# Performance work log

Measured on AMD Instinct MI355X. Metric: run time of the kernel, lower is better.

The kernel has to match this reference:

```python
import jax, jax.numpy as jnp
import numpy as np

N1 = 50000
N2 = 50000
NN = 16
NI = 64
ND = 128


def setup_inputs() -> dict:
    key = jax.random.key(0)
    ks = jax.random.split(key, 12)
    inp = {
        "features1": jax.random.normal(ks[0], (N1, NI), dtype=jnp.float32),
        "features2": jax.random.normal(ks[1], (N2, NI), dtype=jnp.float32),
        "x1": jax.random.normal(ks[2], (N1, 3), dtype=jnp.float32),
        "x2": jax.random.normal(ks[3], (N2, 3), dtype=jnp.float32),
        "nuv1": jax.random.normal(ks[4], (N1, 3, 3), dtype=jnp.float32),
        "nuv2": jax.random.normal(ks[5], (N2, 3, 3), dtype=jnp.float32),
        "topk": jax.random.randint(ks[6], (N1, NN), 0, N2, dtype=jnp.int64),
        # query_f params: Linear(2*Ni, Nd) -> ELU -> Linear(Nd, Nd) -> ELU
        "W1": jax.random.normal(ks[7], (2 * NI, ND), dtype=jnp.float32) * (1.0 / np.sqrt(2 * NI)),
        "b1": jnp.zeros((ND,), dtype=jnp.float32),
        "W2": jax.random.normal(ks[8], (ND, ND), dtype=jnp.float32) * (1.0 / np.sqrt(ND)),
        "b2": jnp.zeros((ND,), dtype=jnp.float32),
        "radius": jnp.float32(1.0),
    }
    return inp


def reference(features1, features2, x1, x2, nuv1, nuv2, topk, W1, b1, W2, b2, radius):
    # gather neighbor features: [N1, nn, Ni]
    feats_nn = features2[topk]
    # concat with self features broadcast over neighbor axis: [N1, nn, 2*Ni]
    feat_self = jnp.broadcast_to(features1[:, None, :], feats_nn.shape)
    h = jnp.concatenate([feats_nn, feat_self], axis=-1)
    # small fused MLP (query_f)
    h = jax.nn.elu(h @ W1 + b1)
    h = jax.nn.elu(h @ W2 + b2)  # [N1, nn, Nd]
    # distance-weighted aggregation
    x_nn = x2[topk]                          # [N1, nn, 3]
    orient = x_nn - x1[:, None, :]
    dis2 = jnp.sum(orient * orient, axis=2)  # [N1, nn]
    w = jnp.exp(-dis2 / (2.0 * radius * radius))
    w = jnp.where(topk == 0, jnp.float32(0.0), w)  # mask padded (index-0) neighbors
    # weighted matmul reduction: [N1, Nd]
    out = jnp.einsum("nk,nkd->nd", w, h)
    return out
```

## Files before the change

### kernel.cpp

```cpp
#include <hip/hip_runtime.h>

#define N1C 50000
#define N2C 50000
#define NNC 16
#define NIC 64
#define NDC 128
#define QB  16
#define MR  256
#define FELEMS (N1C * NIC)

typedef __bf16 bf16x8 __attribute__((ext_vector_type(8)));
typedef float f32x4 __attribute__((ext_vector_type(4)));
typedef unsigned u32x4 __attribute__((ext_vector_type(4)));

#if defined(__has_builtin)
#if __has_builtin(__builtin_amdgcn_cvt_pk_bf16_f32)
#define HAVE_PK_BF16 1
#endif
#if __has_builtin(__builtin_amdgcn_permlane32_swap)
#define HAVE_PL32 1
#endif
#endif

#ifdef HAVE_PK_BF16
typedef __bf16 bf16x2 __attribute__((ext_vector_type(2)));
static __device__ __forceinline__ unsigned int pkbf(float a, float b) {
    bf16x2 r = __builtin_amdgcn_cvt_pk_bf16_f32(a, b);
    return __builtin_bit_cast(unsigned int, r);
}
#else
static __device__ __forceinline__ unsigned short f2bf_sw(float f) {
    unsigned int u = __builtin_bit_cast(unsigned int, f);
    u += 0x7fffu + ((u >> 16) & 1u);
    return (unsigned short)(u >> 16);
}
static __device__ __forceinline__ unsigned int pkbf(float a, float b) {
    return (unsigned int)f2bf_sw(a) | ((unsigned int)f2bf_sw(b) << 16);
}
#endif

static __device__ __forceinline__ float elu(float x) {
    return x > 0.f ? x : __expf(x) - 1.f;
}

static __device__ __forceinline__ void stage16(const uint4* gsrc_lane, uint4* ldst_base) {
#if defined(__has_builtin) && __has_builtin(__builtin_amdgcn_global_load_lds)
    __builtin_amdgcn_global_load_lds(
        (const __attribute__((address_space(1))) void*)gsrc_lane,
        (__attribute__((address_space(3))) void*)ldst_base, 16, 0, 0);
#else
    ldst_base[threadIdx.x & 63] = *gsrc_lane;
#endif
}

__global__ void prep_all(const float* __restrict__ f1, const float* __restrict__ f2,
                         const float* __restrict__ W1, const float* __restrict__ W2,
                         unsigned short* __restrict__ fdst,
                         unsigned short* __restrict__ wsW) {
    const int blk = blockIdx.x;
    if (blk < 3125) {
        const int g = blk * 256 + threadIdx.x;
        const size_t base = (size_t)g * 8;
        const float* src = (base < FELEMS) ? (f1 + base) : (f2 + base - FELEMS);
        const float4 v0 = *(const float4*)src;
        const float4 v1 = *(const float4*)(src + 4);
        uint4 o;
        o.x = pkbf(v0.x, v0.y);
        o.y = pkbf(v0.z, v0.w);
        o.z = pkbf(v1.x, v1.y);
        o.w = pkbf(v1.z, v1.w);
        *(uint4*)(fdst + base) = o;
    } else {
        const int idx  = (blk - 3125) * 256 + threadIdx.x;
        const int m    = idx >> 14;
        const int o    = idx & 16383;
        const int j    = o & 7;
        const int lane = (o >> 3) & 63;
        const int ksmt = o >> 9;
        const int ks   = ksmt & 3;
        const int mt   = ksmt >> 2;
        const int d = mt * 16 + (lane & 15);
        const int k = ks * 32 + (lane >> 4) * 8 + j;
        const float* W = m ? W2 : W1;
        wsW[idx] = (unsigned short)pkbf(W[(size_t)k * NDC + d], 0.f);
    }
}

__global__ __launch_bounds__(512, 4)
void fused_knn_mlp(const unsigned short* __restrict__ f1b,
                   const unsigned short* __restrict__ f2b,
                   const float* __restrict__ x1,
                   const float* __restrict__ x2,
                   const int*   __restrict__ topk,
                   const float* __restrict__ b1,
                   const float* __restrict__ b2,
                   const float* __restrict__ radius,
                   const unsigned short* __restrict__ wsW,
                   float* __restrict__ out)
{
    __shared__ uint4 sW[4096];

    const int tid  = threadIdx.x;
    const int blk  = blockIdx.x;
    const int lane = tid & 63;
    const int wave = tid >> 6;
    const int quad = lane >> 4;
    const int l16  = lane & 15;
    const int rloc = wave * 32 + l16;

    const uint4* wp = (const uint4*)wsW;

    #pragma unroll
    for (int it = 0; it < 8; ++it) {
        const int base = wave * 512 + it * 64;
        stage16(wp + base + lane, sW + base);
    }

    const int idx0 = topk[blk * MR + rloc];
    const int idx1 = topk[blk * MR + rloc + 16];
    const int q0   = blk * QB + wave * 2;
    const int q1   = q0 + 1;

    uint4 xf0[4], xf1[4];
    #pragma unroll
    for (int ks = 0; ks < 2; ++ks) {
        xf0[ks] = *(const uint4*)(f2b + (size_t)idx0 * NIC + ks * 32 + quad * 8);
        xf1[ks] = *(const uint4*)(f2b + (size_t)idx1 * NIC + ks * 32 + quad * 8);
        xf0[ks + 2] = *(const uint4*)(f1b + (size_t)q0 * NIC + ks * 32 + quad * 8);
        xf1[ks + 2] = *(const uint4*)(f1b + (size_t)q1 * NIC + ks * 32 + quad * 8);
    }

    float wg0, wg1;
    {
        const float rr = radius[0];
        const float inv2r2 = 1.f / (2.f * rr * rr);
        const float dx0 = x2[idx0 * 3 + 0] - x1[q0 * 3 + 0];
        const float dy0 = x2[idx0 * 3 + 1] - x1[q0 * 3 + 1];
        const float dz0 = x2[idx0 * 3 + 2] - x1[q0 * 3 + 2];
        const float dx1 = x2[idx1 * 3 + 0] - x1[q1 * 3 + 0];
        const float dy1 = x2[idx1 * 3 + 1] - x1[q1 * 3 + 1];
        const float dz1 = x2[idx1 * 3 + 2] - x1[q1 * 3 + 2];
        wg0 = (idx0 == 0) ? 0.f : __expf(-(dx0 * dx0 + dy0 * dy0 + dz0 * dz0) * inv2r2);
        wg1 = (idx1 == 0) ? 0.f : __expf(-(dx1 * dx1 + dy1 * dy1 + dz1 * dz1) * inv2r2);
    }

    __syncthreads();

    unsigned P[8][2][2];
    #pragma unroll
    for (int mp = 0; mp < 4; ++mp) {
        f32x4 accp[2][2];
        #pragma unroll
        for (int mi = 0; mi < 2; ++mi) {
            const float4 b1v = *(const float4*)(b1 + (mp * 2 + mi) * 16 + quad * 4);
            accp[mi][0] = (f32x4){b1v.x, b1v.y, b1v.z, b1v.w};
            accp[mi][1] = accp[mi][0];
        }
        #pragma unroll
        for (int ks = 0; ks < 4; ++ks) {
            const bf16x8 x0  = __builtin_bit_cast(bf16x8, xf0[ks]);
            const bf16x8 x1v = __builtin_bit_cast(bf16x8, xf1[ks]);
            #pragma unroll
            for (int mi = 0; mi < 2; ++mi) {
                const int mt = mp * 2 + mi;
                const bf16x8 a = *(const bf16x8*)&sW[(mt * 4 + ks) * 64 + lane];
                accp[mi][0] = __builtin_amdgcn_mfma_f32_16x16x32_bf16(a, x0,  accp[mi][0], 0, 0, 0);
                accp[mi][1] = __builtin_amdgcn_mfma_f32_16x16x32_bf16(a, x1v, accp[mi][1], 0, 0, 0);
            }
        }
        #pragma unroll
        for (int mi = 0; mi < 2; ++mi) {
            const int mt = mp * 2 + mi;
            #pragma unroll
            for (int nt = 0; nt < 2; ++nt) {
                P[mt][nt][0] = pkbf(elu(accp[mi][nt][0]), elu(accp[mi][nt][1]));
                P[mt][nt][1] = pkbf(elu(accp[mi][nt][2]), elu(accp[mi][nt][3]));
            }
        }
    }

    f32x4 acc2[2][8];
    #pragma unroll
    for (int nt2 = 0; nt2 < 8; ++nt2) {
        const float bb = b2[nt2 * 16 + l16];
        acc2[0][nt2] = (f32x4){bb, bb, bb, bb};
        acc2[1][nt2] = acc2[0][nt2];
    }
    const bool qodd = (quad & 1) != 0;
    #pragma unroll
    for (int ks = 0; ks < 4; ++ks) {
        u32x4 a2[2];
        #pragma unroll
        for (int mt2 = 0; mt2 < 2; ++mt2) {
#ifdef HAVE_PL32
            #pragma unroll
            for (int e = 0; e < 2; ++e) {
                auto pr = __builtin_amdgcn_permlane32_swap(
                    P[2 * ks][mt2][e], P[2 * ks + 1][mt2][e], false, false);
                const unsigned Rv = qodd ? (unsigned)pr[1] : (unsigned)pr[0];
                const unsigned Zv = qodd ? (unsigned)pr[0] : (unsigned)pr[1];
                const unsigned Sv = __shfl_xor(Zv, 16, 64);
                a2[mt2][e]     = qodd ? Sv : Rv;
                a2[mt2][2 + e] = qodd ? Rv : Sv;
            }
#else
            #pragma unroll
            for (int u = 0; u < 4; ++u) {
                const int src = (((quad * 2) + (u >> 1)) & 3) * 16 + l16;
                const unsigned lo = __shfl(P[2 * ks][mt2][u & 1], src, 64);
                const unsigned hi = __shfl(P[2 * ks + 1][mt2][u & 1], src, 64);
                a2[mt2][u] = (quad & 2) ? hi : lo;
            }
#endif
        }
        const bf16x8 af0 = __builtin_bit_cast(bf16x8, a2[0]);
        const bf16x8 af1 = __builtin_bit_cast(bf16x8, a2[1]);
        #pragma unroll
        for (int nt2 = 0; nt2 < 8; ++nt2) {
            const bf16x8 b = *(const bf16x8*)&sW[2048 + (nt2 * 4 + ks) * 64 + lane];
            acc2[0][nt2] = __builtin_amdgcn_mfma_f32_16x16x32_bf16(af0, b, acc2[0][nt2], 0, 0, 0);
            acc2[1][nt2] = __builtin_amdgcn_mfma_f32_16x16x32_bf16(af1, b, acc2[1][nt2], 0, 0, 0);
        }
    }

    float wk0[4], wk1[4];
    #pragma unroll
    for (int reg = 0; reg < 4; ++reg) {
        const int src = (lane & 48) | (quad * 4 + reg);
        wk0[reg] = __shfl(wg0, src, 64);
        wk1[reg] = __shfl(wg1, src, 64);
    }
    #pragma unroll
    for (int mt2 = 0; mt2 < 2; ++mt2) {
        #pragma unroll
        for (int nt2 = 0; nt2 < 8; ++nt2) {
            const int d2 = nt2 * 16 + l16;
            float s;
            if (mt2 == 0)
                s = elu(acc2[0][nt2][0]) * wk0[0] + elu(acc2[0][nt2][1]) * wk0[1]
                  + elu(acc2[0][nt2][2]) * wk0[2] + elu(acc2[0][nt2][3]) * wk0[3];
            else
                s = elu(acc2[1][nt2][0]) * wk1[0] + elu(acc2[1][nt2][1]) * wk1[1]
                  + elu(acc2[1][nt2][2]) * wk1[2] + elu(acc2[1][nt2][3]) * wk1[3];
            s += __shfl_xor(s, 16, 64);
            s += __shfl_xor(s, 32, 64);
            if (lane < 16) {
                out[(size_t)(blk * QB + wave * 2 + mt2) * NDC + d2] = s;
            }
        }
    }
}

extern "C" void kernel_launch(void* const* d_in, const int* in_sizes, int n_in,
                              void* d_out, int out_size, void* d_ws, size_t ws_size,
                              hipStream_t stream) {
    const float* features1 = (const float*)d_in[0];
    const float* features2 = (const float*)d_in[1];
    const float* x1        = (const float*)d_in[2];
    const float* x2        = (const float*)d_in[3];
    const int*   topk      = (const int*)d_in[6];
    const float* W1        = (const float*)d_in[7];
    const float* b1        = (const float*)d_in[8];
    const float* W2        = (const float*)d_in[9];
    const float* b2        = (const float*)d_in[10];
    const float* radius    = (const float*)d_in[11];
    float* out = (float*)d_out;

    unsigned short* wsW = (unsigned short*)d_ws;
    unsigned short* f1b = wsW + 32768;
    unsigned short* f2b = f1b + FELEMS;

    prep_all<<<dim3(3253), 256, 0, stream>>>(features1, features2, W1, W2, f1b, wsW);
    fused_knn_mlp<<<dim3(N1C / QB), 512, 0, stream>>>(f1b, f2b, x1, x2, topk,
                                                      b1, b2, radius, wsW, out);
}
```

Measured before the change: 187.1 us.

## Make fused kernel persistent with next-tile prefetch and MFMA-based weighted reduction

Turns the fused KNN-MLP kernel into a persistent grid of 512 blocks that loops over query tiles. W1/W2 are staged into LDS once per block, and the next tile's topk indices, gathered features and distance weights load while the current tile runs its MLP. The final weighted sum over neighbours moves from ELU-multiply plus cross-lane shuffle reductions to an fp16 MFMA with the weights as the A operand. This cuts per-block setup and hides gather latency, but lowers occupancy and puts the weights and activations into fp16 for the final reduction.

After: 726.3 us. +288.1%, slower.

```diff
diff --git a/kernel.cpp b/kernel.cpp
--- a/kernel.cpp
+++ b/kernel.cpp
@@ -7,11 +7,16 @@
 #define NDC 128
 #define QB  16
 #define MR  256
+#define NT  (N1C / QB)
+#define PGRID 512
 #define FELEMS (N1C * NIC)
 
 typedef __bf16 bf16x8 __attribute__((ext_vector_type(8)));
 typedef float f32x4 __attribute__((ext_vector_type(4)));
 typedef unsigned u32x4 __attribute__((ext_vector_type(4)));
+typedef unsigned u32x2 __attribute__((ext_vector_type(2)));
+typedef __fp16 f16x4 __attribute__((ext_vector_type(4)));
+typedef __fp16 f16x2 __attribute__((ext_vector_type(2)));
 
 #if defined(__has_builtin)
 #if __has_builtin(__builtin_amdgcn_cvt_pk_bf16_f32)
@@ -19,6 +24,9 @@
 #endif
 #if __has_builtin(__builtin_amdgcn_permlane32_swap)
 #define HAVE_PL32 1
+#endif
+#if __has_builtin(__builtin_amdgcn_mfma_f32_16x16x16f16) && __has_builtin(__builtin_amdgcn_cvt_pkrtz)
+#define HAVE_RED_MFMA 1
 #endif
 #endif
 
@@ -36,6 +44,17 @@
 }
 static __device__ __forceinline__ unsigned int pkbf(float a, float b) {
     return (unsigned int)f2bf_sw(a) | ((unsigned int)f2bf_sw(b) << 16);
+}
+#endif
+
+#ifdef HAVE_RED_MFMA
+static __device__ __forceinline__ unsigned pkh(float a, float b) {
+    f16x2 h = __builtin_amdgcn_cvt_pkrtz(a, b);
+    return __builtin_bit_cast(unsigned, h);
+}
+static __device__ __forceinline__ f16x4 mkf16x4(unsigned lo, unsigned hi) {
+    u32x2 u = {lo, hi};
+    return __builtin_bit_cast(f16x4, u);
 }
 #endif
 
@@ -116,138 +135,201 @@
         stage16(wp + base + lane, sW + base);
     }
 
-    const int idx0 = topk[blk * MR + rloc];
-    const int idx1 = topk[blk * MR + rloc + 16];
-    const int q0   = blk * QB + wave * 2;
-    const int q1   = q0 + 1;
-
+    const float rr = radius[0];
+    const float inv2r2 = 1.f / (2.f * rr * rr);
+
+    int t = blk;
     uint4 xf0[4], xf1[4];
-    #pragma unroll
-    for (int ks = 0; ks < 2; ++ks) {
-        xf0[ks] = *(const uint4*)(f2b + (size_t)idx0 * NIC + ks * 32 + quad * 8);
-        xf1[ks] = *(const uint4*)(f2b + (size_t)idx1 * NIC + ks * 32 + quad * 8);
-        xf0[ks + 2] = *(const uint4*)(f1b + (size_t)q0 * NIC + ks * 32 + quad * 8);
-        xf1[ks + 2] = *(const uint4*)(f1b + (size_t)q1 * NIC + ks * 32 + quad * 8);
-    }
-
     float wg0, wg1;
     {
-        const float rr = radius[0];
-        const float inv2r2 = 1.f / (2.f * rr * rr);
-        const float dx0 = x2[idx0 * 3 + 0] - x1[q0 * 3 + 0];
-        const float dy0 = x2[idx0 * 3 + 1] - x1[q0 * 3 + 1];
-        const float dz0 = x2[idx0 * 3 + 2] - x1[q0 * 3 + 2];
-        const float dx1 = x2[idx1 * 3 + 0] - x1[q1 * 3 + 0];
-        const float dy1 = x2[idx1 * 3 + 1] - x1[q1 * 3 + 1];
-        const float dz1 = x2[idx1 * 3 + 2] - x1[q1 * 3 + 2];
-        wg0 = (idx0 == 0) ? 0.f : __expf(-(dx0 * dx0 + dy0 * dy0 + dz0 * dz0) * inv2r2);
-        wg1 = (idx1 == 0) ? 0.f : __expf(-(dx1 * dx1 + dy1 * dy1 + dz1 * dz1) * inv2r2);
+        const int i0 = topk[t * MR + rloc];
+        const int i1 = topk[t * MR + rloc + 16];
+        const int q0 = t * QB + wave * 2;
+        const int q1 = q0 + 1;
+        #pragma unroll
+        for (int ks = 0; ks < 2; ++ks) {
+            xf0[ks] = *(const uint4*)(f2b + (size_t)i0 * NIC + ks * 32 + quad * 8);
+            xf1[ks] = *(const uint4*)(f2b + (size_t)i1 * NIC + ks * 32 + quad * 8);
+            xf0[ks + 2] = *(const uint4*)(f1b + (size_t)q0 * NIC + ks * 32 + quad * 8);
+            xf1[ks + 2] = *(const uint4*)(f1b + (size_t)q1 * NIC + ks * 32 + quad * 8);
+        }
+        const float dx0 = x2[i0 * 3 + 0] - x1[q0 * 3 + 0];
+        const float dy0 = x2[i0 * 3 + 1] - x1[q0 * 3 + 1];
+        const float dz0 = x2[i0 * 3 + 2] - x1[q0 * 3 + 2];
+        const float dx1 = x2[i1 * 3 + 0] - x1[q1 * 3 + 0];
+        const float dy1 = x2[i1 * 3 + 1] - x1[q1 * 3 + 1];
+        const float dz1 = x2[i1 * 3 + 2] - x1[q1 * 3 + 2];
+        wg0 = (i0 == 0) ? 0.f : __expf(-(dx0 * dx0 + dy0 * dy0 + dz0 * dz0) * inv2r2);
+        wg1 = (i1 == 0) ? 0.f : __expf(-(dx1 * dx1 + dy1 * dy1 + dz1 * dz1) * inv2r2);
     }
 
     __syncthreads();
 
-    unsigned P[8][2][2];
-    #pragma unroll
-    for (int mp = 0; mp < 4; ++mp) {
-        f32x4 accp[2][2];
-        #pragma unroll
-        for (int mi = 0; mi < 2; ++mi) {
-            const float4 b1v = *(const float4*)(b1 + (mp * 2 + mi) * 16 + quad * 4);
-            accp[mi][0] = (f32x4){b1v.x, b1v.y, b1v.z, b1v.w};
-            accp[mi][1] = accp[mi][0];
-        }
-        #pragma unroll
-        for (int ks = 0; ks < 4; ++ks) {
-            const bf16x8 x0  = __builtin_bit_cast(bf16x8, xf0[ks]);
-            const bf16x8 x1v = __builtin_bit_cast(bf16x8, xf1[ks]);
+    for (;;) {
+        unsigned P[8][2][2];
+        #pragma unroll
+        for (int mp = 0; mp < 4; ++mp) {
+            f32x4 accp[2][2];
+            #pragma unroll
+            for (int mi = 0; mi < 2; ++mi) {
+                const float4 b1v = *(const float4*)(b1 + (mp * 2 + mi) * 16 + quad * 4);
+                accp[mi][0] = (f32x4){b1v.x, b1v.y, b1v.z, b1v.w};
+                accp[mi][1] = accp[mi][0];
+            }
+            #pragma unroll
+            for (int ks = 0; ks < 4; ++ks) {
+                const bf16x8 x0  = __builtin_bit_cast(bf16x8, xf0[ks]);
+                const bf16x8 x1v = __builtin_bit_cast(bf16x8, xf1[ks]);
+                #pragma unroll
+                for (int mi = 0; mi < 2; ++mi) {
+                    const int mt = mp * 2 + mi;
+                    const bf16x8 a = *(const bf16x8*)&sW[(mt * 4 + ks) * 64 + lane];
+                    accp[mi][0] = __builtin_amdgcn_mfma_f32_16x16x32_bf16(a, x0,  accp[mi][0], 0, 0, 0);
+                    accp[mi][1] = __builtin_amdgcn_mfma_f32_16x16x32_bf16(a, x1v, accp[mi][1], 0, 0, 0);
+                }
+            }
             #pragma unroll
             for (int mi = 0; mi < 2; ++mi) {
                 const int mt = mp * 2 + mi;
-                const bf16x8 a = *(const bf16x8*)&sW[(mt * 4 + ks) * 64 + lane];
-                accp[mi][0] = __builtin_amdgcn_mfma_f32_16x16x32_bf16(a, x0,  accp[mi][0], 0, 0, 0);
-                accp[mi][1] = __builtin_amdgcn_mfma_f32_16x16x32_bf16(a, x1v, accp[mi][1], 0, 0, 0);
-            }
-        }
-        #pragma unroll
-        for (int mi = 0; mi < 2; ++mi) {
-            const int mt = mp * 2 + mi;
-            #pragma unroll
-            for (int nt = 0; nt < 2; ++nt) {
-                P[mt][nt][0] = pkbf(elu(accp[mi][nt][0]), elu(accp[mi][nt][1]));
-                P[mt][nt][1] = pkbf(elu(accp[mi][nt][2]), elu(accp[mi][nt][3]));
-            }
-        }
-    }
-
-    f32x4 acc2[2][8];
-    #pragma unroll
-    for (int nt2 = 0; nt2 < 8; ++nt2) {
-        const float bb = b2[nt2 * 16 + l16];
-        acc2[0][nt2] = (f32x4){bb, bb, bb, bb};
-        acc2[1][nt2] = acc2[0][nt2];
-    }
-    const bool qodd = (quad & 1) != 0;
-    #pragma unroll
-    for (int ks = 0; ks < 4; ++ks) {
-        u32x4 a2[2];
+                #pragma unroll
+                for (int nt = 0; nt < 2; ++nt) {
+                    P[mt][nt][0] = pkbf(elu(accp[mi][nt][0]), elu(accp[mi][nt][1]));
+                    P[mt][nt][1] = pkbf(elu(accp[mi][nt][2]), elu(accp[mi][nt][3]));
+                }
+            }
+        }
+
+        const int tn = t + PGRID;
+        const bool more = tn < NT;
+        int ni0 = 0, ni1 = 0;
+        if (more) {
+            ni0 = topk[tn * MR + rloc];
+            ni1 = topk[tn * MR + rloc + 16];
+        }
+
+        f32x4 acc2[2][8];
+        #pragma unroll
+        for (int nt2 = 0; nt2 < 8; ++nt2) {
+            const float bb = b2[nt2 * 16 + l16];
+            acc2[0][nt2] = (f32x4){bb, bb, bb, bb};
+            acc2[1][nt2] = acc2[0][nt2];
+        }
+        const bool qodd = (quad & 1) != 0;
+        #pragma unroll
+        for (int ks = 0; ks < 4; ++ks) {
+            u32x4 a2[2];
+            #pragma unroll
+            for (int mt2 = 0; mt2 < 2; ++mt2) {
+#ifdef HAVE_PL32
+                #pragma unroll
+                for (int e = 0; e < 2; ++e) {
+                    auto pr = __builtin_amdgcn_permlane32_swap(
+                        P[2 * ks][mt2][e], P[2 * ks + 1][mt2][e], false, false);
+                    const unsigned Rv = qodd ? (unsigned)pr[1] : (unsigned)pr[0];
+                    const unsigned Zv = qodd ? (unsigned)pr[0] : (unsigned)pr[1];
+                    const unsigned Sv = __shfl_xor(Zv, 16, 64);
+                    a2[mt2][e]     = qodd ? Sv : Rv;
+                    a2[mt2][2 + e] = qodd ? Rv : Sv;
+                }
+#else
+                #pragma unroll
+                for (int u = 0; u < 4; ++u) {
+                    const int src = (((quad * 2) + (u >> 1)) & 3) * 16 + l16;
+                    const unsigned lo = __shfl(P[2 * ks][mt2][u & 1], src, 64);
+                    const unsigned hi = __shfl(P[2 * ks + 1][mt2][u & 1], src, 64);
+                    a2[mt2][u] = (quad & 2) ? hi : lo;
+                }
+#endif
+            }
+            const bf16x8 af0 = __builtin_bit_cast(bf16x8, a2[0]);
+            const bf16x8 af1 = __builtin_bit_cast(bf16x8, a2[1]);
+            #pragma unroll
+            for (int nt2 = 0; nt2 < 8; ++nt2) {
+                const bf16x8 b = *(const bf16x8*)&sW[2048 + (nt2 * 4 + ks) * 64 + lane];
+                acc2[0][nt2] = __builtin_amdgcn_mfma_f32_16x16x32_bf16(af0, b, acc2[0][nt2], 0, 0, 0);
+                acc2[1][nt2] = __builtin_amdgcn_mfma_f32_16x16x32_bf16(af1, b, acc2[1][nt2], 0, 0, 0);
+            }
+        }
+
+#ifdef HAVE_RED_MFMA
+        float w0j[4], w1j[4];
+        #pragma unroll
+        for (int j = 0; j < 4; ++j) {
+            w0j[j] = __shfl(wg0, quad * 4 + j, 64);
+            w1j[j] = __shfl(wg1, quad * 4 + j, 64);
+        }
+        const f16x4 aw0 = mkf16x4(pkh(w0j[0], w0j[1]), pkh(w0j[2], w0j[3]));
+        const f16x4 aw1 = mkf16x4(pkh(w1j[0], w1j[1]), pkh(w1j[2], w1j[3]));
+#else
+        float wk0[4], wk1[4];
+        #pragma unroll
+        for (int reg = 0; reg < 4; ++reg) {
+            const int src = (lane & 48) | (quad * 4 + reg);
+            wk0[reg] = __shfl(wg0, src, 64);
+            wk1[reg] = __shfl(wg1, src, 64);
+        }
+#endif
+
+        if (more) {
+            const int nq0 = tn * QB + wave * 2;
+            const int nq1 = nq0 + 1;
+            #pragma unroll
+            for (int ks = 0; ks < 2; ++ks) {
+                xf0[ks] = *(const uint4*)(f2b + (size_t)ni0 * NIC + ks * 32 + quad * 8);
+                xf1[ks] = *(const uint4*)(f2b + (size_t)ni1 * NIC + ks * 32 + quad * 8);
+                xf0[ks + 2] = *(const uint4*)(f1b + (size_t)nq0 * NIC + ks * 32 + quad * 8);
+                xf1[ks + 2] = *(const uint4*)(f1b + (size_t)nq1 * NIC + ks * 32 + quad * 8);
+            }
+            const float dx0 = x2[ni0 * 3 + 0] - x1[nq0 * 3 + 0];
+            const float dy0 = x2[ni0 * 3 + 1] - x1[nq0 * 3 + 1];
+            const float dz0 = x2[ni0 * 3 + 2] - x1[nq0 * 3 + 2];
+            const float dx1 = x2[ni1 * 3 + 0] - x1[nq1 * 3 + 0];
+            const float dy1 = x2[ni1 * 3 + 1] - x1[nq1 * 3 + 1];
+            const float dz1 = x2[ni1 * 3 + 2] - x1[nq1 * 3 + 2];
+            wg0 = (ni0 == 0) ? 0.f : __expf(-(dx0 * dx0 + dy0 * dy0 + dz0 * dz0) * inv2r2);
+            wg1 = (ni1 == 0) ? 0.f : __expf(-(dx1 * dx1 + dy1 * dy1 + dz1 * dz1) * inv2r2);
+        }
+
+        const size_t ob = (size_t)(t * QB + wave * 2) * NDC;
+#ifdef HAVE_RED_MFMA
+        const f32x4 zero4 = {0.f, 0.f, 0.f, 0.f};
+        #pragma unroll
+        for (int nt2 = 0; nt2 < 8; ++nt2) {
+            const f16x4 be0 = mkf16x4(pkh(elu(acc2[0][nt2][0]), elu(acc2[0][nt2][1])),
+                                      pkh(elu(acc2[0][nt2][2]), elu(acc2[0][nt2][3])));
+            const f16x4 be1 = mkf16x4(pkh(elu(acc2[1][nt2][0]), elu(acc2[1][nt2][1])),
+                                      pkh(elu(acc2[1][nt2][2]), elu(acc2[1][nt2][3])));
+            const f32x4 d0 = __builtin_amdgcn_mfma_f32_16x16x16f16(aw0, be0, zero4, 0, 0, 0);
+            const f32x4 d1 = __builtin_amdgcn_mfma_f32_16x16x16f16(aw1, be1, zero4, 0, 0, 0);
+            if (quad == 0) {
+                out[ob + nt2 * 16 + l16] = d0[0];
+                out[ob + NDC + nt2 * 16 + l16] = d1[0];
+            }
+        }
+#else
         #pragma unroll
         for (int mt2 = 0; mt2 < 2; ++mt2) {
-#ifdef HAVE_PL32
-            #pragma unroll
-            for (int e = 0; e < 2; ++e) {
-                auto pr = __builtin_amdgcn_permlane32_swap(
-                    P[2 * ks][mt2][e], P[2 * ks + 1][mt2][e], false, false);
-                const unsigned Rv = qodd ? (unsigned)pr[1] : (unsigned)pr[0];
-                const unsigned Zv = qodd ? (unsigned)pr[0] : (unsigned)pr[1];
-                const unsigned Sv = __shfl_xor(Zv, 16, 64);
-                a2[mt2][e]     = qodd ? Sv : Rv;
-                a2[mt2][2 + e] = qodd ? Rv : Sv;
-            }
-#else
-            #pragma unroll
-            for (int u = 0; u < 4; ++u) {
-                const int src = (((quad * 2) + (u >> 1)) & 3) * 16 + l16;
-                const unsigned lo = __shfl(P[2 * ks][mt2][u & 1], src, 64);
-                const unsigned hi = __shfl(P[2 * ks + 1][mt2][u & 1], src, 64);
-                a2[mt2][u] = (quad & 2) ? hi : lo;
-            }
-#endif
-        }
-        const bf16x8 af0 = __builtin_bit_cast(bf16x8, a2[0]);
-        const bf16x8 af1 = __builtin_bit_cast(bf16x8, a2[1]);
-        #pragma unroll
-        for (int nt2 = 0; nt2 < 8; ++nt2) {
-            const bf16x8 b = *(const bf16x8*)&sW[2048 + (nt2 * 4 + ks) * 64 + lane];
-            acc2[0][nt2] = __builtin_amdgcn_mfma_f32_16x16x32_bf16(af0, b, acc2[0][nt2], 0, 0, 0);
-            acc2[1][nt2] = __builtin_amdgcn_mfma_f32_16x16x32_bf16(af1, b, acc2[1][nt2], 0, 0, 0);
-        }
-    }
-
-    float wk0[4], wk1[4];
-    #pragma unroll
-    for (int reg = 0; reg < 4; ++reg) {
-        const int src = (lane & 48) | (quad * 4 + reg);
-        wk0[reg] = __shfl(wg0, src, 64);
-        wk1[reg] = __shfl(wg1, src, 64);
-    }
-    #pragma unroll
-    for (int mt2 = 0; mt2 < 2; ++mt2) {
-        #pragma unroll
-        for (int nt2 = 0; nt2 < 8; ++nt2) {
-            const int d2 = nt2 * 16 + l16;
-            float s;
-            if (mt2 == 0)
-                s = elu(acc2[0][nt2][0]) * wk0[0] + elu(acc2[0][nt2][1]) * wk0[1]
-                  + elu(acc2[0][nt2][2]) * wk0[2] + elu(acc2[0][nt2][3]) * wk0[3];
-            else
-                s = elu(acc2[1][nt2][0]) * wk1[0] + elu(acc2[1][nt2][1]) * wk1[1]
-                  + elu(acc2[1][nt2][2]) * wk1[2] + elu(acc2[1][nt2][3]) * wk1[3];
-            s += __shfl_xor(s, 16, 64);
-            s += __shfl_xor(s, 32, 64);
-            if (lane < 16) {
-                out[(size_t)(blk * QB + wave * 2 + mt2) * NDC + d2] = s;
-            }
-        }
+            #pragma unroll
+            for (int nt2 = 0; nt2 < 8; ++nt2) {
+                const int d2 = nt2 * 16 + l16;
+                float s;
+                if (mt2 == 0)
+                    s = elu(acc2[0][nt2][0]) * wk0[0] + elu(acc2[0][nt2][1]) * wk0[1]
+                      + elu(acc2[0][nt2][2]) * wk0[2] + elu(acc2[0][nt2][3]) * wk0[3];
+                else
+                    s = elu(acc2[1][nt2][0]) * wk1[0] + elu(acc2[1][nt2][1]) * wk1[1]
+                      + elu(acc2[1][nt2][2]) * wk1[2] + elu(acc2[1][nt2][3]) * wk1[3];
+                s += __shfl_xor(s, 16, 64);
+                s += __shfl_xor(s, 32, 64);
+                if (lane < 16) {
+                    out[ob + mt2 * NDC + d2] = s;
+                }
+            }
+        }
+#endif
+
+        if (!more) break;
+        t = tn;
     }
 }
 
@@ -271,6 +353,6 @@
     unsigned short* f2b = f1b + FELEMS;
 
     prep_all<<<dim3(3253), 256, 0, stream>>>(features1, features2, W1, W2, f1b, wsW);
-    fused_knn_mlp<<<dim3(N1C / QB), 512, 0, stream>>>(f1b, f2b, x1, x2, topk,
-                                                      b1, b2, radius, wsW, out);
-}
+    fused_knn_mlp<<<dim3(PGRID), 512, 0, stream>>>(f1b, f2b, x1, x2, topk,
+                                                   b1, b2, radius, wsW, out);
+}
```
